# Performance work log

Measured on AMD Instinct MI355X. Metric: run time of the kernel, lower is better.

## Reference

```python
import jax, jax.numpy as jnp
import numpy as np

K = 16          # filter order (number of Laplacian powers)
MLP_OUT = 16    # mlp_hid == mlp_out for mlp_nlayers == 1
D_PE = 64       # phi output dim
BN_EPS = 1e-5
B, N, M = 8, 1024, 128
E = 131072


def setup_inputs() -> dict:
    key = jax.random.key(0)
    ks = jax.random.split(key, 12)
    # Symmetric, spectrally-bounded Laplacian surrogate so 15 matrix powers stay finite.
    A = jax.random.normal(ks[0], (B, N, N), dtype=jnp.float32)
    Lap = (A + jnp.swapaxes(A, -1, -2)) * (0.5 / jnp.sqrt(jnp.float32(N)))
    W = jax.random.normal(ks[1], (B, N, M), dtype=jnp.float32)
    edge_index = jax.random.randint(ks[2], (2, E), 0, B * N, dtype=jnp.int64)
    batch = jnp.repeat(jnp.arange(B, dtype=jnp.int64), N)
    # MLP layer (k -> MLP_OUT) + BatchNorm affine params
    lin_w = jax.random.normal(ks[3], (K, MLP_OUT), dtype=jnp.float32) / jnp.sqrt(jnp.float32(K))
    lin_b = jnp.zeros((MLP_OUT,), dtype=jnp.float32)
    bn_gamma = jnp.ones((MLP_OUT,), dtype=jnp.float32)
    bn_beta = jnp.zeros((MLP_OUT,), dtype=jnp.float32)
    # phi: GIN-style 2-layer MLP after neighbor aggregation
    phi_w1 = jax.random.normal(ks[4], (MLP_OUT, D_PE), dtype=jnp.float32) / jnp.sqrt(jnp.float32(MLP_OUT))
    phi_b1 = jnp.zeros((D_PE,), dtype=jnp.float32)
    phi_w2 = jax.random.normal(ks[5], (D_PE, D_PE), dtype=jnp.float32) / jnp.sqrt(jnp.float32(D_PE))
    phi_b2 = jnp.zeros((D_PE,), dtype=jnp.float32)
    return {"Lap": Lap, "W": W, "lin_w": lin_w, "lin_b": lin_b,
            "bn_gamma": bn_gamma, "bn_beta": bn_beta,
            "phi_w1": phi_w1, "phi_b1": phi_b1, "phi_w2": phi_w2, "phi_b2": phi_b2,
            "edge_index": edge_index, "batch": batch}


def _filter(S, W0):
    """Sequential power filter: returns [k, N, M] = [W0, S@W0, S^2@W0, ...]."""
    def step(out, _):
        nxt = S @ out
        return nxt, nxt
    _, rest = jax.lax.scan(step, W0, None, length=K - 1)
    return jnp.concatenate([W0[None], rest], axis=0)


def reference(Lap, W, lin_w, lin_b, bn_gamma, bn_beta,
              phi_w1, phi_b1, phi_w2, phi_b2, edge_index, batch):
    # Batched filter over all graphs: [B, k, N, M] -> [B, N, M, k]
    feat = jax.vmap(_filter)(Lap, W)
    feat = jnp.transpose(feat, (0, 2, 3, 1))
    # Linear over k -> MLP_OUT channels: [B, N, M, C]
    h = feat @ lin_w + lin_b
    # BatchNorm1d (training mode), per-graph statistics over (N, M) per channel,
    # matching the torch per-graph loop where BN sees [M, C, N].
    mean = jnp.mean(h, axis=(1, 2), keepdims=True)
    var = jnp.var(h, axis=(1, 2), keepdims=True)
    h = (h - mean) * jax.lax.rsqrt(var + BN_EPS) * bn_gamma + bn_beta
    h = jax.nn.relu(h)
    # phi: pool random-sample dim M, flatten graphs -> [N_sum, C]
    x = jnp.mean(h, axis=2).reshape(-1, h.shape[-1])
    src, dst = edge_index[0], edge_index[1]
    agg = jax.ops.segment_sum(x[src], dst, num_segments=x.shape[0])
    g = x + agg  # GIN aggregation
    out = jax.nn.relu(g @ phi_w1 + phi_b1) @ phi_w2 + phi_b2  # [N_sum, D_PE]
    return out
```

## Files before the change

### kernel.cpp

```cpp
#include <hip/hip_runtime.h>

#define B 8
#define N 1024
#define M 128
#define KF 16
#define C 16
#define DPE 64
#define NE 131072
#define NV (B*N)
#define NM (N*M)
#define BN_EPS 1e-5f

typedef short bf16x8 __attribute__((ext_vector_type(8)));
typedef float f32x4 __attribute__((ext_vector_type(4)));

__device__ inline unsigned short f2bf_rne(float f) {
    unsigned u = __float_as_uint(f);
    u += 0x7fffu + ((u >> 16) & 1u);
    return (unsigned short)(u >> 16);
}
__device__ inline float bf2f(unsigned short s) {
    return __uint_as_float((unsigned)s << 16);
}
__device__ inline void split_bf16(float v, unsigned short& hi, unsigned short& lo) {
    hi = f2bf_rne(v);
    float hf = __uint_as_float((unsigned)hi << 16);
    lo = f2bf_rne(v - hf);
}
union U4 { uint4 v; unsigned short s[8]; };
union U2 { uint2 v; unsigned short s[4]; };

__device__ __host__ inline size_t SF4(int b, int nsub, int ks, int hl, int l) {
    return ((((size_t)b * 64 + nsub) * 32 + ks) * 2 + hl) * 64 + l;
}
__device__ __host__ inline size_t PF4(int b, int msub, int ks, int hl, int l) {
    return ((((size_t)b * 8 + msub) * 32 + ks) * 2 + hl) * 64 + l;
}
#define PFBUF ((size_t)B * 8 * 32 * 2 * 64)

__global__ __launch_bounds__(256) void prep_all(const float* __restrict__ Lap,
                                                const float* __restrict__ W,
                                                const int* __restrict__ ei,
                                                uint4* __restrict__ Sf,
                                                uint4* __restrict__ Pf,
                                                unsigned short* __restrict__ feat,
                                                int* __restrict__ cnt) {
    __shared__ float T[32][33];
    int blk = blockIdx.x;
    int t = threadIdx.x;
    if (blk < 512) {
        int b = blk & 7, nb = blk >> 3;
        int nl = t >> 4, kg = t & 15;
        int n = nb * 16 + nl;
        const float* row = Lap + ((size_t)b * N + n) * N;
        #pragma unroll
        for (int jj = 0; jj < 8; jj++) {
            int koct = kg + 16 * jj;
            int k0 = koct * 8;
            float4 f0 = *(const float4*)(row + k0);
            float4 f1 = *(const float4*)(row + k0 + 4);
            float e[8] = {f0.x, f0.y, f0.z, f0.w, f1.x, f1.y, f1.z, f1.w};
            U4 hi, lo;
            #pragma unroll
            for (int j = 0; j < 8; j++) split_bf16(e[j], hi.s[j], lo.s[j]);
            int ks = k0 >> 5;
            int lf = nl + 16 * (koct & 3);
            Sf[SF4(b, nb, ks, 0, lf)] = hi.v;
            Sf[SF4(b, nb, ks, 1, lf)] = lo.v;
        }
    } else if (blk < 1536) {
        int r = blk - 512;
        int b = r & 7;
        int tile = r >> 3;
        int nt = tile & 31, mt = tile >> 5;
        int n0 = nt * 32, m0 = mt * 32;
        {
            int nl = t >> 3, mq = t & 7;
            float4 v = *(const float4*)(W + ((size_t)b * N + n0 + nl) * M + m0 + mq * 4);
            T[nl][mq * 4 + 0] = v.x; T[nl][mq * 4 + 1] = v.y;
            T[nl][mq * 4 + 2] = v.z; T[nl][mq * 4 + 3] = v.w;
        }
        __syncthreads();
        {
            int ml = t >> 3, nq = t & 7;
            U2 o;
            o.s[0] = f2bf_rne(T[nq * 4 + 0][ml]);
            o.s[1] = f2bf_rne(T[nq * 4 + 1][ml]);
            o.s[2] = f2bf_rne(T[nq * 4 + 2][ml]);
            o.s[3] = f2bf_rne(T[nq * 4 + 3][ml]);
            unsigned short* plane = feat + (size_t)b * KF * NM;
            *(uint2*)(plane + (size_t)(m0 + ml) * N + n0 + nq * 4) = o.v;
        }
    } else if (blk < 2048) {
        int r0 = blk - 1536;
        int b = r0 & 7;
        int r = (r0 >> 3) * 256 + t;
        int msub = r >> 11, ks = (r >> 6) & 31, l = r & 63;
        int m = 16 * msub + (l & 15);
        U4 hi, lo;
        #pragma unroll
        for (int j = 0; j < 8; j++) {
            int n = 32 * ks + 8 * (l >> 4) + j;
            float v = W[((size_t)b * N + n) * M + m];
            split_bf16(v, hi.s[j], lo.s[j]);
        }
        Pf[PF4(b, msub, ks, 0, l)] = hi.v;
        Pf[PF4(b, msub, ks, 1, l)] = lo.v;
    } else {
        int e = (blk - 2048) * 256 + t;
        bool is64 = (ei[1] == 0 && ei[3] == 0 && ei[5] == 0 && ei[7] == 0);
        int dst = is64 ? ei[2 * (NE + e)] : ei[NE + e];
        atomicAdd(&cnt[dst], 1);
    }
}

__global__ __launch_bounds__(512) void gemm_chain(const uint4* __restrict__ Sf,
                                                  uint4* __restrict__ PfA,
                                                  uint4* __restrict__ PfB,
                                                  unsigned short* __restrict__ feat,
                                                  unsigned* bar) {
    extern __shared__ __align__(16) char smem[];
    uint4* ldsS = (uint4*)smem;
    float* Dl = (float*)(smem + 131072);

    int b = blockIdx.x & 7, bx = blockIdx.x >> 3;
    int t = threadIdx.x;
    int w = t >> 6, lane = t & 63;
    int g = w >> 2, wq = w & 3;
    int rot = bx & 15;
    size_t sbase = SF4(b, 2 * bx, 0, 0, 0);
    int n0 = 32 * bx;

    #pragma unroll
    for (int i = 0; i < 16; i++) ldsS[t + 512 * i] = Sf[sbase + t + 512 * i];
    __syncthreads();

    #pragma unroll 1
    for (int k = 0; k < KF - 1; k++) {
        const uint4* PfIn = (k & 1) ? PfB : PfA;
        uint4* PfOut      = (k & 1) ? PfA : PfB;
        const uint4* Pw0 = PfIn + (size_t)(b * 8 + 2 * wq) * 4096 + (size_t)(16 * g) * 128;
        const uint4* Pw1 = Pw0 + 4096;

        f32x4 acc[2][2] = {};
        uint4 ph[4][2], pl[4][2];
        #pragma unroll
        for (int q = 0; q < 4; q++) {
            int ke = (q + rot) & 15;
            ph[q][0] = Pw0[(size_t)ke * 128 + lane];
            pl[q][0] = Pw0[(size_t)ke * 128 + 64 + lane];
            ph[q][1] = Pw1[(size_t)ke * 128 + lane];
            pl[q][1] = Pw1[(size_t)ke * 128 + 64 + lane];
        }
        #pragma unroll
        for (int ks = 0; ks < 16; ks++) {
            int slot = ks & 3;
            int kg = 16 * g + ((ks + rot) & 15);
            uint4 a0h = ph[slot][0], a0l = pl[slot][0];
            uint4 a1h = ph[slot][1], a1l = pl[slot][1];
            if (ks < 12) {
                int kn = (ks + 4 + rot) & 15;
                ph[slot][0] = Pw0[(size_t)kn * 128 + lane];
                pl[slot][0] = Pw0[(size_t)kn * 128 + 64 + lane];
                ph[slot][1] = Pw1[(size_t)kn * 128 + lane];
                pl[slot][1] = Pw1[(size_t)kn * 128 + 64 + lane];
            }
            bf16x8 b0h = __builtin_bit_cast(bf16x8, ldsS[kg * 128 + lane]);
            bf16x8 b0l = __builtin_bit_cast(bf16x8, ldsS[kg * 128 + 64 + lane]);
            bf16x8 b1h = __builtin_bit_cast(bf16x8, ldsS[4096 + kg * 128 + lane]);
            bf16x8 b1l = __builtin_bit_cast(bf16x8, ldsS[4096 + kg * 128 + 64 + lane]);
            bf16x8 A0h = __builtin_bit_cast(bf16x8, a0h);
            bf16x8 A0l = __builtin_bit_cast(bf16x8, a0l);
            bf16x8 A1h = __builtin_bit_cast(bf16x8, a1h);
            bf16x8 A1l = __builtin_bit_cast(bf16x8, a1l);
            acc[0][0] = __builtin_amdgcn_mfma_f32_16x16x32_bf16(A0h, b0h, acc[0][0], 0, 0, 0);
            acc[0][0] = __builtin_amdgcn_mfma_f32_16x16x32_bf16(A0h, b0l, acc[0][0], 0, 0, 0);
            acc[0][0] = __builtin_amdgcn_mfma_f32_16x16x32_bf16(A0l, b0h, acc[0][0], 0, 0, 0);
            acc[0][1] = __builtin_amdgcn_mfma_f32_16x16x32_bf16(A0h, b1h, acc[0][1], 0, 0, 0);
            acc[0][1] = __builtin_amdgcn_mfma_f32_16x16x32_bf16(A0h, b1l, acc[0][1], 0, 0, 0);
            acc[0][1] = __builtin_amdgcn_mfma_f32_16x16x32_bf16(A0l, b1h, acc[0][1], 0, 0, 0);
            acc[1][0] = __builtin_amdgcn_mfma_f32_16x16x32_bf16(A1h, b0h, acc[1][0], 0, 0, 0);
            acc[1][0] = __builtin_amdgcn_mfma_f32_16x16x32_bf16(A1h, b0l, acc[1][0], 0, 0, 0);
            acc[1][0] = __builtin_amdgcn_mfma_f32_16x16x32_bf16(A1l, b0h, acc[1][0], 0, 0, 0);
            acc[1][1] = __builtin_amdgcn_mfma_f32_16x16x32_bf16(A1h, b1h, acc[1][1], 0, 0, 0);
            acc[1][1] = __builtin_amdgcn_mfma_f32_16x16x32_bf16(A1h, b1l, acc[1][1], 0, 0, 0);
            acc[1][1] = __builtin_amdgcn_mfma_f32_16x16x32_bf16(A1l, b1h, acc[1][1], 0, 0, 0);
        }

        if (g == 1) {
            #pragma unroll
            for (int mi = 0; mi < 2; mi++)
                #pragma unroll
                for (int ni = 0; ni < 2; ni++)
                    #pragma unroll
                    for (int r = 0; r < 4; r++) {
                        int m = 32 * wq + 16 * mi + 4 * (lane >> 4) + r;
                        int c = 16 * ni + (lane & 15);
                        Dl[m * 36 + c] = acc[mi][ni][r];
                    }
        }
        __syncthreads();
        if (g == 0) {
            #pragma unroll
            for (int mi = 0; mi < 2; mi++)
                #pragma unroll
                for (int ni = 0; ni < 2; ni++)
                    #pragma unroll
                    for (int r = 0; r < 4; r++) {
                        int m = 32 * wq + 16 * mi + 4 * (lane >> 4) + r;
                        int c = 16 * ni + (lane & 15);
                        Dl[m * 36 + c] += acc[mi][ni][r];
                    }
        }
        __syncthreads();
        if (k < KF - 2) {
            {
                int l = t & 63;
                int m = 16 * w + (l & 15);
                int ncol = 8 * (l >> 4);
                float4 v0 = *(const float4*)&Dl[m * 36 + ncol];
                float4 v1 = *(const float4*)&Dl[m * 36 + ncol + 4];
                float e[8] = {v0.x, v0.y, v0.z, v0.w, v1.x, v1.y, v1.z, v1.w};
                U4 hi, lo;
                #pragma unroll
                for (int j = 0; j < 8; j++) split_bf16(e[j], hi.s[j], lo.s[j]);
                PfOut[PF4(b, w, bx, 0, l)] = hi.v;
                PfOut[PF4(b, w, bx, 1, l)] = lo.v;
            }
            __syncthreads();
            if (t == 0)
                __hip_atomic_fetch_add(&bar[b * 32], 1u, __ATOMIC_RELAXED,
                                       __HIP_MEMORY_SCOPE_AGENT);
            {
                int m = t >> 2, c0 = (t & 3) * 8;
                U4 o;
                #pragma unroll
                for (int j = 0; j < 8; j++) o.s[j] = f2bf_rne(Dl[m * 36 + c0 + j]);
                unsigned short* plane = feat + ((size_t)b * KF + (k + 1)) * NM + (size_t)m * N + n0 + c0;
                *(uint4*)plane = o.v;
            }
            if (t == 0) {
                unsigned target = 32u * (unsigned)(k + 1);
                while (__hip_atomic_load(&bar[b * 32], __ATOMIC_RELAXED,
                                         __HIP_MEMORY_SCOPE_AGENT) < target)
                    __builtin_amdgcn_s_sleep(1);
            }
            __syncthreads();
            asm volatile("buffer_inv sc0\n\ts_waitcnt vmcnt(0)" ::: "memory");
        } else {
            int m = t >> 2, c0 = (t & 3) * 8;
            U4 o;
            #pragma unroll
            for (int j = 0; j < 8; j++) o.s[j] = f2bf_rne(Dl[m * 36 + c0 + j]);
            unsigned short* plane = feat + ((size_t)b * KF + (k + 1)) * NM + (size_t)m * N + n0 + c0;
            *(uint4*)plane = o.v;
        }
    }
}

__global__ __launch_bounds__(256) void bn_stats_scan(const unsigned short* __restrict__ feat,
                                                     const float* __restrict__ lin_w,
                                                     const float* __restrict__ lin_b,
                                                     float* __restrict__ stats,
                                                     const int* __restrict__ cnt,
                                                     int* __restrict__ off,
                                                     int* __restrict__ cur) {
    __shared__ float wls[KF * C];
    __shared__ float red[4][2][C];
    __shared__ int ss[256];
    int t = threadIdx.x;
    if (blockIdx.x < 8) {
        if (blockIdx.x == 0) {
            int base = t * 32;
            int local[32];
            int s = 0;
            #pragma unroll
            for (int i = 0; i < 32; i++) { local[i] = cnt[base + i]; s += local[i]; }
            ss[t] = s;
            __syncthreads();
            #pragma unroll
            for (int d = 1; d < 256; d <<= 1) {
                int v = (t >= d) ? ss[t - d] : 0;
                __syncthreads();
                ss[t] += v;
                __syncthreads();
            }
            int excl = ss[t] - s;
            #pragma unroll
            for (int i = 0; i < 32; i++) { off[base + i] = excl; cur[base + i] = excl; excl += local[i]; }
        }
        return;
    }
    int blk = blockIdx.x - 8;
    wls[t] = lin_w[t];
    __syncthreads();
    int b = blk & 7;
    int i = (blk >> 3) * 256 + t;
    const uint2* fb = (const uint2*)(feat + (size_t)b * KF * NM);

    float4 hacc[C];
    #pragma unroll
    for (int c = 0; c < C; c++) {
        float bb = lin_b[c];
        hacc[c] = make_float4(bb, bb, bb, bb);
    }
    for (int kk = 0; kk < KF; kk++) {
        U2 u; u.v = fb[(size_t)kk * (NM / 4) + i];
        float p0 = bf2f(u.s[0]), p1 = bf2f(u.s[1]), p2 = bf2f(u.s[2]), p3 = bf2f(u.s[3]);
        #pragma unroll
        for (int c = 0; c < C; c++) {
            float wv = wls[kk * C + c];
            hacc[c].x = fmaf(p0, wv, hacc[c].x);
            hacc[c].y = fmaf(p1, wv, hacc[c].y);
            hacc[c].z = fmaf(p2, wv, hacc[c].z);
            hacc[c].w = fmaf(p3, wv, hacc[c].w);
        }
    }
    float s[C], ssq[C];
    #pragma unroll
    for (int c = 0; c < C; c++) {
        float4 h = hacc[c];
        s[c] = h.x + h.y + h.z + h.w;
        ssq[c] = h.x * h.x + h.y * h.y + h.z * h.z + h.w * h.w;
    }
    #pragma unroll
    for (int o = 32; o > 0; o >>= 1)
        #pragma unroll
        for (int c = 0; c < C; c++) {
            s[c] += __shfl_down(s[c], o);
            ssq[c] += __shfl_down(ssq[c], o);
        }
    if ((t & 63) == 0) {
        int wv = t >> 6;
        #pragma unroll
        for (int c = 0; c < C; c++) { red[wv][0][c] = s[c]; red[wv][1][c] = ssq[c]; }
    }
    __syncthreads();
    if (t < 32) {
        int which = t >> 4, c = t & 15;
        float v = red[0][which][c] + red[1][which][c] + red[2][which][c] + red[3][which][c];
        atomicAdd(&stats[b * 32 + which * 16 + c], v);
    }
}

__global__ __launch_bounds__(256) void bnx_fill(const unsigned short* __restrict__ feat,
                                                const float* __restrict__ lin_w,
                                                const float* __restrict__ lin_b,
                                                const float* __restrict__ gam,
                                                const float* __restrict__ bet,
                                                const float* __restrict__ stats,
                                                float* __restrict__ x,
                                                const int* __restrict__ ei,
                                                int* __restrict__ cur,
                                                int* __restrict__ bucket) {
    __shared__ float wls[KF * C];
    __shared__ float red[8][32 * 17];
    int t = threadIdx.x;
    if (blockIdx.x >= 256) {
        int e = (blockIdx.x - 256) * 256 + t;
        bool is64 = (ei[1] == 0 && ei[3] == 0 && ei[5] == 0 && ei[7] == 0);
        int src, dst;
        if (is64) { src = ei[2 * e]; dst = ei[2 * (NE + e)]; }
        else      { src = ei[e];     dst = ei[NE + e]; }
        int pos = atomicAdd(&cur[dst], 1);
        bucket[pos] = src;
        return;
    }
    wls[t] = lin_w[t];
    __syncthreads();
    int grp = blockIdx.x;
    int b = grp & 7, n0 = (grp >> 3) * 32;
    int nl = t & 31, mg = t >> 5;
    int n = n0 + nl;

    const float inv_nm = 1.0f / (float)NM;
    float sc[C], sh[C], bb[C];
    #pragma unroll
    for (int c = 0; c < C; c++) {
        float mean = stats[b * 32 + c] * inv_nm;
        float var = stats[b * 32 + 16 + c] * inv_nm - mean * mean;
        sc[c] = gam[c] * rsqrtf(var + BN_EPS);
        sh[c] = bet[c] - mean * sc[c];
        bb[c] = lin_b[c];
    }
    const unsigned short* fb = feat + (size_t)b * KF * NM + n;
    float y[C] = {};
    for (int m = mg * 16; m < mg * 16 + 16; m++) {
        float p[KF];
        #pragma unroll
        for (int kk = 0; kk < KF; kk++) p[kk] = bf2f(fb[(size_t)kk * NM + (size_t)m * N]);
        #pragma unroll
        for (int c = 0; c < C; c++) {
            float h = bb[c];
            #pragma unroll
            for (int kk = 0; kk < KF; kk++) h = fmaf(p[kk], wls[kk * C + c], h);
            y[c] += fmaxf(fmaf(h, sc[c], sh[c]), 0.0f);
        }
    }
    #pragma unroll
    for (int c = 0; c < C; c++) red[mg][nl * 17 + c] = y[c];
    __syncthreads();
    #pragma unroll
    for (int q = 0; q < 2; q++) {
        int slot = t + q * 256;
        int snl = slot >> 4, c = slot & 15;
        float v = 0.0f;
        #pragma unroll
        for (int m8 = 0; m8 < 8; m8++) v += red[m8][snl * 17 + c];
        v *= (1.0f / (float)M);
        x[((size_t)b * N + n0 + snl) * C + c] = v;
    }
}

__global__ __launch_bounds__(256) void phi_fused(const int* __restrict__ cnt,
                                                 const int* __restrict__ off,
                                                 const int* __restrict__ bucket,
                                                 const float* __restrict__ x,
                                                 const float* __restrict__ w1,
                                                 const float* __restrict__ b1,
                                                 const float* __restrict__ w2,
                                                 const float* __restrict__ b2,
                                                 float* __restrict__ out) {
    __shared__ float w1s[C * DPE];
    __shared__ float w2s[DPE * DPE];
    __shared__ float b2s[DPE];
    __shared__ float gsh[16][17];
    __shared__ float h1sh[16][DPE];
    int t = threadIdx.x;
    #pragma unroll
    for (int q = 0; q < 4; q++) w1s[t + q * 256] = w1[t + q * 256];
    #pragma unroll
    for (int q = 0; q < 16; q++) w2s[t + q * 256] = w2[t + q * 256];
    if (t < DPE) b2s[t] = b2[t];

    {
        int nl = t >> 4, c = t & 15;
        int n = blockIdx.x * 16 + nl;
        int o = off[n], d = cnt[n];
        float v = x[(size_t)n * C + c];
        int j = 0;
        for (; j + 4 <= d; j += 4) {
            int s0 = bucket[o + j], s1 = bucket[o + j + 1];
            int s2 = bucket[o + j + 2], s3 = bucket[o + j + 3];
            v += x[(size_t)s0 * C + c];
            v += x[(size_t)s1 * C + c];
            v += x[(size_t)s2 * C + c];
            v += x[(size_t)s3 * C + c];
        }
        for (; j < d; j++) v += x[(size_t)bucket[o + j] * C + c];
        gsh[nl][c] = v;
    }
    __syncthreads();
    #pragma unroll
    for (int q = 0; q < 4; q++) {
        int item = t + 256 * q;
        int node = item >> 6, j = item & 63;
        float h = b1[j];
        #pragma unroll
        for (int c = 0; c < C; c++) h = fmaf(gsh[node][c], w1s[c * DPE + j], h);
        h1sh[node][j] = fmaxf(h, 0.0f);
    }
    __syncthreads();
    #pragma unroll
    for (int q = 0; q < 4; q++) {
        int item = t + 256 * q;
        int node = item >> 6, d = item & 63;
        float o2 = b2s[d];
        #pragma unroll
        for (int j = 0; j < DPE; j++) o2 = fmaf(h1sh[node][j], w2s[j * DPE + d], o2);
        out[((size_t)blockIdx.x * 16 + node) * DPE + d] = o2;
    }
}

extern "C" void kernel_launch(void* const* d_in, const int* in_sizes, int n_in,
                              void* d_out, int out_size, void* d_ws, size_t ws_size,
                              hipStream_t stream) {
    const float* Lap   = (const float*)d_in[0];
    const float* W     = (const float*)d_in[1];
    const float* lin_w = (const float*)d_in[2];
    const float* lin_b = (const float*)d_in[3];
    const float* gam   = (const float*)d_in[4];
    const float* bet   = (const float*)d_in[5];
    const float* w1    = (const float*)d_in[6];
    const float* b1    = (const float*)d_in[7];
    const float* w2    = (const float*)d_in[8];
    const float* b2    = (const float*)d_in[9];
    const int*   ei    = (const int*)d_in[10];

    char* wsb = (char*)d_ws;
    unsigned short* feat = (unsigned short*)wsb;
    uint4* Sf    = (uint4*)(wsb + ((size_t)32 << 20));
    uint4* Pf    = (uint4*)(wsb + ((size_t)64 << 20));
    char* tail   = wsb + ((size_t)72 << 20);
    float* stats = (float*)tail;
    unsigned* bar = (unsigned*)(tail + 1024);
    int* cnt     = (int*)(tail + 8192);
    float* x     = (float*)(tail + 40960);
    int* off     = (int*)(x + (size_t)NV * C);
    int* cur     = off + NV;
    int* bucket  = cur + NV;
    float* out   = (float*)d_out;

    static bool attr_set = false;
    if (!attr_set) {
        hipFuncSetAttribute((const void*)gemm_chain,
                            hipFuncAttributeMaxDynamicSharedMemorySize, 149504);
        attr_set = true;
    }

    hipMemsetAsync(tail, 0, 40960, stream);
    prep_all<<<dim3(2560), 256, 0, stream>>>(Lap, W, ei, Sf, Pf, feat, cnt);
    gemm_chain<<<dim3(256), 512, 149504, stream>>>(Sf, Pf, Pf + PFBUF, feat, bar);
    bn_stats_scan<<<dim3(1032), 256, 0, stream>>>(feat, lin_w, lin_b, stats, cnt, off, cur);
    bnx_fill<<<dim3(768), 256, 0, stream>>>(feat, lin_w, lin_b, gam, bet, stats, x, ei, cur, bucket);
    phi_fused<<<dim3(NV / 16), 256, 0, stream>>>(cnt, off, bucket, x, w1, b1, w2, b2, out);
}
```

Measured before the change: 293.8 us.

## Use per-wave grid barrier arrivals and register-cache first LDS filter tiles

Replaces the block-level arrive/wait (one thread per block, two extra __syncthreads) with per-wave arrivals on the grid barrier counter, so each wave publishes its slice and spins on its own. The feat output is now written from the bf16 high half computed for the Pf split, which drops a second conversion pass. The first four k-steps' Laplacian B-fragments are kept in registers across iterations, and MFMA bursts are wrapped in s_setprio. The costs are more register pressure, eight times more atomics and spinning waves per block, and an added __syncthreads before the reduction.

After: 704.6 us. 140% more time.

```diff
diff --git a/kernel.cpp b/kernel.cpp
--- a/kernel.cpp
+++ b/kernel.cpp
@@ -135,6 +135,19 @@
     for (int i = 0; i < 16; i++) ldsS[t + 512 * i] = Sf[sbase + t + 512 * i];
     __syncthreads();
 
+    uint4 bp[16];
+    #pragma unroll
+    for (int q = 0; q < 4; q++) {
+        int kg = 16 * g + ((q + rot) & 15);
+        bp[4 * q + 0] = ldsS[kg * 128 + lane];
+        bp[4 * q + 1] = ldsS[kg * 128 + 64 + lane];
+        bp[4 * q + 2] = ldsS[4096 + kg * 128 + lane];
+        bp[4 * q + 3] = ldsS[4096 + kg * 128 + 64 + lane];
+    }
+
+    int cm = 16 * w + (lane & 15);
+    int cn = 8 * (lane >> 4);
+
     #pragma unroll 1
     for (int k = 0; k < KF - 1; k++) {
         const uint4* PfIn = (k & 1) ? PfB : PfA;
@@ -165,14 +178,23 @@
                 ph[slot][1] = Pw1[(size_t)kn * 128 + lane];
                 pl[slot][1] = Pw1[(size_t)kn * 128 + 64 + lane];
             }
-            bf16x8 b0h = __builtin_bit_cast(bf16x8, ldsS[kg * 128 + lane]);
-            bf16x8 b0l = __builtin_bit_cast(bf16x8, ldsS[kg * 128 + 64 + lane]);
-            bf16x8 b1h = __builtin_bit_cast(bf16x8, ldsS[4096 + kg * 128 + lane]);
-            bf16x8 b1l = __builtin_bit_cast(bf16x8, ldsS[4096 + kg * 128 + 64 + lane]);
+            bf16x8 b0h, b0l, b1h, b1l;
+            if (ks < 4) {
+                b0h = __builtin_bit_cast(bf16x8, bp[4 * ks + 0]);
+                b0l = __builtin_bit_cast(bf16x8, bp[4 * ks + 1]);
+                b1h = __builtin_bit_cast(bf16x8, bp[4 * ks + 2]);
+                b1l = __builtin_bit_cast(bf16x8, bp[4 * ks + 3]);
+            } else {
+                b0h = __builtin_bit_cast(bf16x8, ldsS[kg * 128 + lane]);
+                b0l = __builtin_bit_cast(bf16x8, ldsS[kg * 128 + 64 + lane]);
+                b1h = __builtin_bit_cast(bf16x8, ldsS[4096 + kg * 128 + lane]);
+                b1l = __builtin_bit_cast(bf16x8, ldsS[4096 + kg * 128 + 64 + lane]);
+            }
             bf16x8 A0h = __builtin_bit_cast(bf16x8, a0h);
             bf16x8 A0l = __builtin_bit_cast(bf16x8, a0l);
             bf16x8 A1h = __builtin_bit_cast(bf16x8, a1h);
             bf16x8 A1l = __builtin_bit_cast(bf16x8, a1l);
+            __builtin_amdgcn_s_setprio(1);
             acc[0][0] = __builtin_amdgcn_mfma_f32_16x16x32_bf16(A0h, b0h, acc[0][0], 0, 0, 0);
             acc[0][0] = __builtin_amdgcn_mfma_f32_16x16x32_bf16(A0h, b0l, acc[0][0], 0, 0, 0);
             acc[0][0] = __builtin_amdgcn_mfma_f32_16x16x32_bf16(A0l, b0h, acc[0][0], 0, 0, 0);
@@ -185,8 +207,10 @@
             acc[1][1] = __builtin_amdgcn_mfma_f32_16x16x32_bf16(A1h, b1h, acc[1][1], 0, 0, 0);
             acc[1][1] = __builtin_amdgcn_mfma_f32_16x16x32_bf16(A1h, b1l, acc[1][1], 0, 0, 0);
             acc[1][1] = __builtin_amdgcn_mfma_f32_16x16x32_bf16(A1l, b1h, acc[1][1], 0, 0, 0);
-        }
-
+            __builtin_amdgcn_s_setprio(0);
+        }
+
+        __syncthreads();
         if (g == 1) {
             #pragma unroll
             for (int mi = 0; mi < 2; mi++)
@@ -213,47 +237,32 @@
                     }
         }
         __syncthreads();
-        if (k < KF - 2) {
-            {
-                int l = t & 63;
-                int m = 16 * w + (l & 15);
-                int ncol = 8 * (l >> 4);
-                float4 v0 = *(const float4*)&Dl[m * 36 + ncol];
-                float4 v1 = *(const float4*)&Dl[m * 36 + ncol + 4];
-                float e[8] = {v0.x, v0.y, v0.z, v0.w, v1.x, v1.y, v1.z, v1.w};
-                U4 hi, lo;
-                #pragma unroll
-                for (int j = 0; j < 8; j++) split_bf16(e[j], hi.s[j], lo.s[j]);
-                PfOut[PF4(b, w, bx, 0, l)] = hi.v;
-                PfOut[PF4(b, w, bx, 1, l)] = lo.v;
-            }
-            __syncthreads();
-            if (t == 0)
-                __hip_atomic_fetch_add(&bar[b * 32], 1u, __ATOMIC_RELAXED,
-                                       __HIP_MEMORY_SCOPE_AGENT);
-            {
-                int m = t >> 2, c0 = (t & 3) * 8;
-                U4 o;
-                #pragma unroll
-                for (int j = 0; j < 8; j++) o.s[j] = f2bf_rne(Dl[m * 36 + c0 + j]);
-                unsigned short* plane = feat + ((size_t)b * KF + (k + 1)) * NM + (size_t)m * N + n0 + c0;
-                *(uint4*)plane = o.v;
-            }
-            if (t == 0) {
-                unsigned target = 32u * (unsigned)(k + 1);
+
+        {
+            float4 v0 = *(const float4*)&Dl[cm * 36 + cn];
+            float4 v1 = *(const float4*)&Dl[cm * 36 + cn + 4];
+            float e[8] = {v0.x, v0.y, v0.z, v0.w, v1.x, v1.y, v1.z, v1.w};
+            U4 hi, lo;
+            #pragma unroll
+            for (int j = 0; j < 8; j++) split_bf16(e[j], hi.s[j], lo.s[j]);
+            unsigned short* plane = feat + ((size_t)b * KF + (k + 1)) * NM
+                                        + (size_t)cm * N + n0 + cn;
+            if (k < KF - 2) {
+                PfOut[PF4(b, w, bx, 0, lane)] = hi.v;
+                PfOut[PF4(b, w, bx, 1, lane)] = lo.v;
+                asm volatile("s_waitcnt vmcnt(0)" ::: "memory");
+                if (lane == 0)
+                    __hip_atomic_fetch_add(&bar[b * 32], 1u, __ATOMIC_RELAXED,
+                                           __HIP_MEMORY_SCOPE_AGENT);
+                *(uint4*)plane = hi.v;
+                unsigned target = 256u * (unsigned)(k + 1);
                 while (__hip_atomic_load(&bar[b * 32], __ATOMIC_RELAXED,
                                          __HIP_MEMORY_SCOPE_AGENT) < target)
                     __builtin_amdgcn_s_sleep(1);
+                asm volatile("buffer_inv sc0\n\ts_waitcnt vmcnt(0)" ::: "memory");
+            } else {
+                *(uint4*)plane = hi.v;
             }
-            __syncthreads();
-            asm volatile("buffer_inv sc0\n\ts_waitcnt vmcnt(0)" ::: "memory");
-        } else {
-            int m = t >> 2, c0 = (t & 3) * 8;
-            U4 o;
-            #pragma unroll
-            for (int j = 0; j < 8; j++) o.s[j] = f2bf_rne(Dl[m * 36 + c0 + j]);
-            unsigned short* plane = feat + ((size_t)b * KF + (k + 1)) * NM + (size_t)m * N + n0 + c0;
-            *(uint4*)plane = o.v;
         }
     }
 }
```

## Split power-chain GEMM into 512 smaller blocks with 16-column tiles, no k-split

Applied to the files above, without the earlier changes.

The persistent power-iteration kernel is restructured from 256 blocks of 512 threads, each owning 32 output columns with a two-group split over the reduction dimension, to 512 blocks of 256 threads, each owning 16 columns with the full reduction done per wave. This removes the cross-group LDS reduction and one barrier per step, halves LDS per block so two blocks can share a CU, and fuses the bf16 feature write with the hi/lo split. The cost is twice as many blocks taking part in the per-graph global spin barrier, and each block re-reads the full P operand from global memory. It also drops the staggered rotation of the reduction index that spread reads across blocks.

Result: slower. 375.3 us (+27.7%).

```diff
diff --git a/kernel.cpp b/kernel.cpp
--- a/kernel.cpp
+++ b/kernel.cpp
@@ -114,146 +114,103 @@
     }
 }
 
-__global__ __launch_bounds__(512) void gemm_chain(const uint4* __restrict__ Sf,
-                                                  uint4* __restrict__ PfA,
-                                                  uint4* __restrict__ PfB,
-                                                  unsigned short* __restrict__ feat,
-                                                  unsigned* bar) {
+__global__ __launch_bounds__(256, 2) void gemm_chain(const uint4* __restrict__ Sf,
+                                                     uint4* __restrict__ PfA,
+                                                     uint4* __restrict__ PfB,
+                                                     unsigned short* __restrict__ feat,
+                                                     unsigned* bar) {
     extern __shared__ __align__(16) char smem[];
     uint4* ldsS = (uint4*)smem;
-    float* Dl = (float*)(smem + 131072);
+    float* Dl   = (float*)(smem + 65536);
 
     int b = blockIdx.x & 7, bx = blockIdx.x >> 3;
     int t = threadIdx.x;
     int w = t >> 6, lane = t & 63;
-    int g = w >> 2, wq = w & 3;
-    int rot = bx & 15;
-    size_t sbase = SF4(b, 2 * bx, 0, 0, 0);
-    int n0 = 32 * bx;
-
-    #pragma unroll
-    for (int i = 0; i < 16; i++) ldsS[t + 512 * i] = Sf[sbase + t + 512 * i];
+    int n0 = 16 * bx;
+    size_t sbase = SF4(b, bx, 0, 0, 0);
+
+    #pragma unroll
+    for (int i = 0; i < 16; i++) ldsS[t + 256 * i] = Sf[sbase + t + 256 * i];
     __syncthreads();
 
     #pragma unroll 1
     for (int k = 0; k < KF - 1; k++) {
         const uint4* PfIn = (k & 1) ? PfB : PfA;
         uint4* PfOut      = (k & 1) ? PfA : PfB;
-        const uint4* Pw0 = PfIn + (size_t)(b * 8 + 2 * wq) * 4096 + (size_t)(16 * g) * 128;
+        const uint4* Pw0 = PfIn + (size_t)(b * 8 + 2 * w) * 4096;
         const uint4* Pw1 = Pw0 + 4096;
 
-        f32x4 acc[2][2] = {};
-        uint4 ph[4][2], pl[4][2];
-        #pragma unroll
-        for (int q = 0; q < 4; q++) {
-            int ke = (q + rot) & 15;
-            ph[q][0] = Pw0[(size_t)ke * 128 + lane];
-            pl[q][0] = Pw0[(size_t)ke * 128 + 64 + lane];
-            ph[q][1] = Pw1[(size_t)ke * 128 + lane];
-            pl[q][1] = Pw1[(size_t)ke * 128 + 64 + lane];
-        }
-        #pragma unroll
-        for (int ks = 0; ks < 16; ks++) {
-            int slot = ks & 3;
-            int kg = 16 * g + ((ks + rot) & 15);
+        f32x4 acc0 = {}, acc1 = {};
+        uint4 ph[2][2], pl[2][2];
+        #pragma unroll
+        for (int q = 0; q < 2; q++) {
+            ph[q][0] = Pw0[(size_t)q * 128 + lane];
+            pl[q][0] = Pw0[(size_t)q * 128 + 64 + lane];
+            ph[q][1] = Pw1[(size_t)q * 128 + lane];
+            pl[q][1] = Pw1[(size_t)q * 128 + 64 + lane];
+        }
+        #pragma unroll
+        for (int ks = 0; ks < 32; ks++) {
+            int slot = ks & 1;
             uint4 a0h = ph[slot][0], a0l = pl[slot][0];
             uint4 a1h = ph[slot][1], a1l = pl[slot][1];
-            if (ks < 12) {
-                int kn = (ks + 4 + rot) & 15;
-                ph[slot][0] = Pw0[(size_t)kn * 128 + lane];
-                pl[slot][0] = Pw0[(size_t)kn * 128 + 64 + lane];
-                ph[slot][1] = Pw1[(size_t)kn * 128 + lane];
-                pl[slot][1] = Pw1[(size_t)kn * 128 + 64 + lane];
+            if (ks < 30) {
+                ph[slot][0] = Pw0[(size_t)(ks + 2) * 128 + lane];
+                pl[slot][0] = Pw0[(size_t)(ks + 2) * 128 + 64 + lane];
+                ph[slot][1] = Pw1[(size_t)(ks + 2) * 128 + lane];
+                pl[slot][1] = Pw1[(size_t)(ks + 2) * 128 + 64 + lane];
             }
-            bf16x8 b0h = __builtin_bit_cast(bf16x8, ldsS[kg * 128 + lane]);
-            bf16x8 b0l = __builtin_bit_cast(bf16x8, ldsS[kg * 128 + 64 + lane]);
-            bf16x8 b1h = __builtin_bit_cast(bf16x8, ldsS[4096 + kg * 128 + lane]);
-            bf16x8 b1l = __builtin_bit_cast(bf16x8, ldsS[4096 + kg * 128 + 64 + lane]);
+            bf16x8 bh = __builtin_bit_cast(bf16x8, ldsS[ks * 128 + lane]);
+            bf16x8 bl = __builtin_bit_cast(bf16x8, ldsS[ks * 128 + 64 + lane]);
             bf16x8 A0h = __builtin_bit_cast(bf16x8, a0h);
             bf16x8 A0l = __builtin_bit_cast(bf16x8, a0l);
             bf16x8 A1h = __builtin_bit_cast(bf16x8, a1h);
             bf16x8 A1l = __builtin_bit_cast(bf16x8, a1l);
-            acc[0][0] = __builtin_amdgcn_mfma_f32_16x16x32_bf16(A0h, b0h, acc[0][0], 0, 0, 0);
-            acc[0][0] = __builtin_amdgcn_mfma_f32_16x16x32_bf16(A0h, b0l, acc[0][0], 0, 0, 0);
-            acc[0][0] = __builtin_amdgcn_mfma_f32_16x16x32_bf16(A0l, b0h, acc[0][0], 0, 0, 0);
-            acc[0][1] = __builtin_amdgcn_mfma_f32_16x16x32_bf16(A0h, b1h, acc[0][1], 0, 0, 0);
-            acc[0][1] = __builtin_amdgcn_mfma_f32_16x16x32_bf16(A0h, b1l, acc[0][1], 0, 0, 0);
-            acc[0][1] = __builtin_amdgcn_mfma_f32_16x16x32_bf16(A0l, b1h, acc[0][1], 0, 0, 0);
-            acc[1][0] = __builtin_amdgcn_mfma_f32_16x16x32_bf16(A1h, b0h, acc[1][0], 0, 0, 0);
-            acc[1][0] = __builtin_amdgcn_mfma_f32_16x16x32_bf16(A1h, b0l, acc[1][0], 0, 0, 0);
-            acc[1][0] = __builtin_amdgcn_mfma_f32_16x16x32_bf16(A1l, b0h, acc[1][0], 0, 0, 0);
-            acc[1][1] = __builtin_amdgcn_mfma_f32_16x16x32_bf16(A1h, b1h, acc[1][1], 0, 0, 0);
-            acc[1][1] = __builtin_amdgcn_mfma_f32_16x16x32_bf16(A1h, b1l, acc[1][1], 0, 0, 0);
-            acc[1][1] = __builtin_amdgcn_mfma_f32_16x16x32_bf16(A1l, b1h, acc[1][1], 0, 0, 0);
-        }
-
-        if (g == 1) {
-            #pragma unroll
-            for (int mi = 0; mi < 2; mi++)
-                #pragma unroll
-                for (int ni = 0; ni < 2; ni++)
-                    #pragma unroll
-                    for (int r = 0; r < 4; r++) {
-                        int m = 32 * wq + 16 * mi + 4 * (lane >> 4) + r;
-                        int c = 16 * ni + (lane & 15);
-                        Dl[m * 36 + c] = acc[mi][ni][r];
-                    }
+            acc0 = __builtin_amdgcn_mfma_f32_16x16x32_bf16(A0h, bh, acc0, 0, 0, 0);
+            acc0 = __builtin_amdgcn_mfma_f32_16x16x32_bf16(A0h, bl, acc0, 0, 0, 0);
+            acc0 = __builtin_amdgcn_mfma_f32_16x16x32_bf16(A0l, bh, acc0, 0, 0, 0);
+            acc1 = __builtin_amdgcn_mfma_f32_16x16x32_bf16(A1h, bh, acc1, 0, 0, 0);
+            acc1 = __builtin_amdgcn_mfma_f32_16x16x32_bf16(A1h, bl, acc1, 0, 0, 0);
+            acc1 = __builtin_amdgcn_mfma_f32_16x16x32_bf16(A1l, bh, acc1, 0, 0, 0);
+        }
+
+        #pragma unroll
+        for (int r = 0; r < 4; r++) {
+            int m0r = 32 * w + 4 * (lane >> 4) + r;
+            Dl[m0r * 20 + (lane & 15)] = acc0[r];
+            Dl[(m0r + 16) * 20 + (lane & 15)] = acc1[r];
         }
         __syncthreads();
-        if (g == 0) {
-            #pragma unroll
-            for (int mi = 0; mi < 2; mi++)
-                #pragma unroll
-                for (int ni = 0; ni < 2; ni++)
-                    #pragma unroll
-                    for (int r = 0; r < 4; r++) {
-                        int m = 32 * wq + 16 * mi + 4 * (lane >> 4) + r;
-                        int c = 16 * ni + (lane & 15);
-                        Dl[m * 36 + c] += acc[mi][ni][r];
-                    }
-        }
-        __syncthreads();
+
+        {
+            int m = t >> 1, half = t & 1;
+            float4 v0 = *(const float4*)&Dl[m * 20 + 8 * half];
+            float4 v1 = *(const float4*)&Dl[m * 20 + 8 * half + 4];
+            float e[8] = {v0.x, v0.y, v0.z, v0.w, v1.x, v1.y, v1.z, v1.w};
+            U4 hi, lo;
+            #pragma unroll
+            for (int j = 0; j < 8; j++) split_bf16(e[j], hi.s[j], lo.s[j]);
+            unsigned short* plane = feat + ((size_t)b * KF + (k + 1)) * NM
+                                        + (size_t)m * N + n0 + 8 * half;
+            *(uint4*)plane = hi.v;
+            if (k < KF - 2) {
+                int l = (m & 15) + 16 * (2 * (bx & 1) + half);
+                PfOut[PF4(b, m >> 4, bx >> 1, 0, l)] = hi.v;
+                PfOut[PF4(b, m >> 4, bx >> 1, 1, l)] = lo.v;
+            }
+        }
         if (k < KF - 2) {
-            {
-                int l = t & 63;
-                int m = 16 * w + (l & 15);
-                int ncol = 8 * (l >> 4);
-                float4 v0 = *(const float4*)&Dl[m * 36 + ncol];
-                float4 v1 = *(const float4*)&Dl[m * 36 + ncol + 4];
-                float e[8] = {v0.x, v0.y, v0.z, v0.w, v1.x, v1.y, v1.z, v1.w};
-                U4 hi, lo;
-                #pragma unroll
-                for (int j = 0; j < 8; j++) split_bf16(e[j], hi.s[j], lo.s[j]);
-                PfOut[PF4(b, w, bx, 0, l)] = hi.v;
-                PfOut[PF4(b, w, bx, 1, l)] = lo.v;
-            }
             __syncthreads();
-            if (t == 0)
+            if (t == 0) {
                 __hip_atomic_fetch_add(&bar[b * 32], 1u, __ATOMIC_RELAXED,
                                        __HIP_MEMORY_SCOPE_AGENT);
-            {
-                int m = t >> 2, c0 = (t & 3) * 8;
-                U4 o;
-                #pragma unroll
-                for (int j = 0; j < 8; j++) o.s[j] = f2bf_rne(Dl[m * 36 + c0 + j]);
-                unsigned short* plane = feat + ((size_t)b * KF + (k + 1)) * NM + (size_t)m * N + n0 + c0;
-                *(uint4*)plane = o.v;
-            }
-            if (t == 0) {
-                unsigned target = 32u * (unsigned)(k + 1);
+                unsigned target = 64u * (unsigned)(k + 1);
                 while (__hip_atomic_load(&bar[b * 32], __ATOMIC_RELAXED,
                                          __HIP_MEMORY_SCOPE_AGENT) < target)
                     __builtin_amdgcn_s_sleep(1);
             }
             __syncthreads();
             asm volatile("buffer_inv sc0\n\ts_waitcnt vmcnt(0)" ::: "memory");
-        } else {
-            int m = t >> 2, c0 = (t & 3) * 8;
-            U4 o;
-            #pragma unroll
-            for (int j = 0; j < 8; j++) o.s[j] = f2bf_rne(Dl[m * 36 + c0 + j]);
-            unsigned short* plane = feat + ((size_t)b * KF + (k + 1)) * NM + (size_t)m * N + n0 + c0;
-            *(uint4*)plane = o.v;
         }
     }
 }
@@ -504,13 +461,13 @@
     static bool attr_set = false;
     if (!attr_set) {
         hipFuncSetAttribute((const void*)gemm_chain,
-                            hipFuncAttributeMaxDynamicSharedMemorySize, 149504);
+                            hipFuncAttributeMaxDynamicSharedMemorySize, 75776);
         attr_set = true;
     }
 
     hipMemsetAsync(tail, 0, 40960, stream);
     prep_all<<<dim3(2560), 256, 0, stream>>>(Lap, W, ei, Sf, Pf, feat, cnt);
-    gemm_chain<<<dim3(256), 512, 149504, stream>>>(Sf, Pf, Pf + PFBUF, feat, bar);
+    gemm_chain<<<dim3(512), 256, 75776, stream>>>(Sf, Pf, Pf + PFBUF, feat, bar);
     bn_stats_scan<<<dim3(1032), 256, 0, stream>>>(feat, lin_w, lin_b, stats, cnt, off, cur);
     bnx_fill<<<dim3(768), 256, 0, stream>>>(feat, lin_w, lin_b, gam, bet, stats, x, ei, cur, bucket);
     phi_fused<<<dim3(NV / 16), 256, 0, stream>>>(cnt, off, bucket, x, w1, b1, w2, b2, out);
```
